# Kernel tuning notes

Measured on AMD Instinct MI355X. Metric: run time of the kernel, lower is better.

## Reference

```python
import jax, jax.numpy as jnp
import numpy as np
from jax import lax

B, T, V, LAT, U, P = 256, 128, 42, 200, 512, 3  # batch, seq, vocab, latent, lstm units, num_prop


def setup_inputs() -> dict:
    key = jax.random.key(0)
    ks = jax.random.split(key, 40)
    g = lambda i, shape, s=0.05: (jax.random.normal(ks[i], shape, jnp.float32) * s)
    inp = {
        'X': jax.random.randint(ks[0], (B, T), 0, V, jnp.int64 if jax.config.jax_enable_x64 else jnp.int32),
        'Y': jax.random.randint(ks[1], (B, T), 0, V, jnp.int32),
        'C': jax.random.normal(ks[2], (B, P), jnp.float32),
        'L': jax.random.randint(ks[3], (B,), 1, T + 1, jnp.int32),
        'eps': jax.random.normal(ks[4], (B, LAT), jnp.float32),
        'emb_enc': g(5, (V, LAT), 0.1),
        'emb_dec': g(6, (V, LAT), 0.1),
        # encoder stacked LSTM: layer0 input dim = LAT + P, layers 1-2 input dim = U
        'enc_k0': g(7, (LAT + P, 4 * U)), 'enc_rk0': g(8, (U, 4 * U)), 'enc_b0': jnp.zeros((4 * U,), jnp.float32),
        'enc_k1': g(9, (U, 4 * U)), 'enc_rk1': g(10, (U, 4 * U)), 'enc_b1': jnp.zeros((4 * U,), jnp.float32),
        'enc_k2': g(11, (U, 4 * U)), 'enc_rk2': g(12, (U, 4 * U)), 'enc_b2': jnp.zeros((4 * U,), jnp.float32),
        # decoder stacked LSTM: layer0 input dim = 2*LAT + P
        'dec_k0': g(13, (2 * LAT + P, 4 * U)), 'dec_rk0': g(14, (U, 4 * U)), 'dec_b0': jnp.zeros((4 * U,), jnp.float32),
        'dec_k1': g(15, (U, 4 * U)), 'dec_rk1': g(16, (U, 4 * U)), 'dec_b1': jnp.zeros((4 * U,), jnp.float32),
        'dec_k2': g(17, (U, 4 * U)), 'dec_rk2': g(18, (U, 4 * U)), 'dec_b2': jnp.zeros((4 * U,), jnp.float32),
        'Wm': g(19, (U, LAT)), 'bm': jnp.zeros((LAT,), jnp.float32),
        'Ws': g(20, (U, LAT)), 'bs': jnp.zeros((LAT,), jnp.float32),
        'Wo': g(21, (U, V)), 'bo': jnp.zeros((V,), jnp.float32),
    }
    return inp


def _lstm_step(x, h, c, k, rk, b):
    # Keras LSTMCell gate order: i, f, g(candidate), o
    z = x @ k + h @ rk + b
    i, f, gg, o = jnp.split(z, 4, axis=-1)
    c2 = jax.nn.sigmoid(f) * c + jax.nn.sigmoid(i) * jnp.tanh(gg)
    h2 = jax.nn.sigmoid(o) * jnp.tanh(c2)
    return h2, c2


def _run_stacked(inp, params):
    # inp: [B, T, D]; params: list of 3 (kernel, recurrent_kernel, bias)
    b = inp.shape[0]
    init = tuple((jnp.zeros((b, U), inp.dtype), jnp.zeros((b, U), inp.dtype)) for _ in range(3))

    def scan_fn(carry, x_t):
        h_in = x_t
        new = []
        for (h, c), (k, rk, bb) in zip(carry, params):
            h2, c2 = _lstm_step(h_in, h, c, k, rk, bb)
            new.append((h2, c2))
            h_in = h2
        return tuple(new), h_in

    carry, ys = lax.scan(scan_fn, init, jnp.swapaxes(inp, 0, 1))
    return jnp.swapaxes(ys, 0, 1), carry  # [B,T,U], final states


def reference(X, Y, C, L, eps, emb_enc, emb_dec,
              enc_k0, enc_rk0, enc_b0, enc_k1, enc_rk1, enc_b1, enc_k2, enc_rk2, enc_b2,
              dec_k0, dec_rk0, dec_b0, dec_k1, dec_rk1, dec_b1, dec_k2, dec_rk2, dec_b2,
              Wm, bm, Ws, bs, Wo, bo):
    enc_params = [(enc_k0, enc_rk0, enc_b0), (enc_k1, enc_rk1, enc_b1), (enc_k2, enc_rk2, enc_b2)]
    dec_params = [(dec_k0, dec_rk0, dec_b0), (dec_k1, dec_rk1, dec_b1), (dec_k2, dec_rk2, dec_b2)]

    # ---- encode ----
    Xe = emb_enc[X]                                       # [B,T,LAT]
    Ct = jnp.broadcast_to(C[:, None, :], (B, T, P))
    enc_in = jnp.concatenate([Xe, Ct], axis=-1)           # [B,T,LAT+P]
    _, enc_states = _run_stacked(enc_in, enc_params)
    h = enc_states[-1][1]                                 # CELL state of last layer (state[-1][1])
    mean = h @ Wm + bm
    log_sigma = h @ Ws + bs
    z = mean + jnp.exp(log_sigma / 2.0) * eps             # [B,LAT]

    # ---- decode ----
    Zt = jnp.broadcast_to(z[:, None, :], (B, T, LAT))
    Xd = emb_dec[X]
    dec_in = jnp.concatenate([Zt, Xd, Ct], axis=-1)       # [B,T,2*LAT+P]
    dec_out, _ = _run_stacked(dec_in, dec_params)
    pre = dec_out @ Wo + bo                               # pre-softmax logits [B,T,V]

    # ---- losses ----
    logp = jax.nn.log_softmax(pre, axis=-1)
    ce = -jnp.take_along_axis(logp, Y[..., None].astype(jnp.int32), axis=-1)[..., 0]  # [B,T]
    weights = (jnp.arange(T)[None, :] < L[:, None]).astype(jnp.float32)
    recon = jnp.mean(ce * weights)
    latent = -0.5 * jnp.mean(1.0 + log_sigma - jnp.square(mean) - jnp.exp(log_sigma))
    loss = recon + latent
    return loss, recon, latent
```

## Files before the change

### kernel.cpp

```cpp
#include <hip/hip_runtime.h>

#define B_ 256
#define T_ 128
#define V_ 42
#define LAT_ 200
#define U_ 512
#define G4_ 2048
#define NBLK 196
#define FI(r, m) ((((r) * 2) + (m)) * 32)
#define SLOT_ ((size_t)B_ * U_)
#define LS_ ((size_t)129 * SLOT_)

typedef unsigned short ushort_t;
typedef __attribute__((ext_vector_type(8))) short bf8;
typedef __attribute__((ext_vector_type(4))) float f4;

__device__ __forceinline__ ushort_t f2bf(float f) {
  union { float f; unsigned int i; } v; v.f = f;
  unsigned int r = v.i + 0x7fffu + ((v.i >> 16) & 1u);
  return (ushort_t)(r >> 16);
}
__device__ __forceinline__ float sigf(float x) { return 1.f / (1.f + __expf(-x)); }
__device__ __forceinline__ float tanhfast(float x) {
  float e = __expf(2.f * x);
  return 1.f - 2.f / (e + 1.f);
}
__device__ __forceinline__ void wait_vm0() {
  asm volatile("s_waitcnt vmcnt(0)" ::: "memory");
}

__global__ __launch_bounds__(256) void table_kernel(const float* emb, const float* k0, int roff, float* table) {
  int v = blockIdx.x, tid = threadIdx.x;
  __shared__ float e[LAT_];
  for (int i = tid; i < LAT_; i += 256) e[i] = emb[v * LAT_ + i];
  __syncthreads();
  for (int j = tid; j < G4_; j += 256) {
    float s = 0.f;
    for (int n = 0; n < LAT_; n++) s += e[n] * k0[(size_t)(roff + n) * G4_ + j];
    table[v * G4_ + j] = s;
  }
}

__device__ __forceinline__ size_t mat_off_u4(int m) {
  if (m == 0) return 0;
  if (m == 1) return 147456;
  if (m < 10) return 360448 + (size_t)(m - 2) * 131072;
  return 1409024;
}

struct SwzSrc {
  const float *enc_rk0, *enc_k0, *enc_b0;
  const float *dec_rk0, *dec_k0, *dec_b0;
  const float *tabE, *tabD;
  const float *encK1, *encR1, *encK2, *encR2;
  const float *decK1, *decR1, *decK2, *decR2;
  const float *Wo;
  ushort_t* dst;
};

__device__ float swz_val(const SwzSrc& s, int mat, int k, int n) {
  switch (mat) {
    case 0: {
      if (k < 512) return s.enc_rk0[(size_t)k * G4_ + n];
      int i = k - 512;
      if (i < 42) return s.tabE[(size_t)i * G4_ + n];
      if (i < 45) return s.enc_k0[(size_t)(200 + i - 42) * G4_ + n];
      if (i == 45) return s.enc_b0[n];
      return 0.f;
    }
    case 1: {
      if (k < 512) return s.dec_rk0[(size_t)k * G4_ + n];
      int i = k - 512;
      if (i < 200) return s.dec_k0[(size_t)i * G4_ + n];
      if (i < 256) return 0.f;
      i -= 256;
      if (i < 42) return s.tabD[(size_t)i * G4_ + n];
      if (i < 45) return s.dec_k0[(size_t)(400 + i - 42) * G4_ + n];
      if (i == 45) return s.dec_b0[n];
      return 0.f;
    }
    case 2: return s.encK1[(size_t)k * G4_ + n];
    case 3: return s.encR1[(size_t)k * G4_ + n];
    case 4: return s.encK2[(size_t)k * G4_ + n];
    case 5: return s.encR2[(size_t)k * G4_ + n];
    case 6: return s.decK1[(size_t)k * G4_ + n];
    case 7: return s.decR1[(size_t)k * G4_ + n];
    case 8: return s.decK2[(size_t)k * G4_ + n];
    case 9: return s.decR2[(size_t)k * G4_ + n];
    default: return (n < V_) ? s.Wo[(size_t)k * V_ + n] : 0.f;
  }
}

__global__ __launch_bounds__(256) void swz_ext_kernel(SwzSrc s) {
  int b = blockIdx.x, tid = threadIdx.x;
  int mat, nt16;
  if (b < 1280) { mat = b >> 7; nt16 = b & 127; } else { mat = 10; nt16 = b - 1280; }
  int ktMax = (mat == 0) ? 18 : (mat == 1) ? 26 : 16;
  int lane = tid & 63, l15 = lane & 15, q = lane >> 4;
  int n = nt16 * 16 + l15;
  uint4* dst = (uint4*)s.dst;
  size_t off = mat_off_u4(mat);
  for (int kt = tid >> 6; kt < ktMax; kt += 4) {
    ushort_t o[8];
    int kb = kt * 32 + q * 8;
#pragma unroll
    for (int j = 0; j < 8; j++) o[j] = f2bf(swz_val(s, mat, kb + j, n));
    dst[off + ((size_t)nt16 * ktMax + kt) * 64 + lane] = *(const uint4*)o;
  }
}

struct PP {
  const ushort_t* swz;
  ushort_t* ring;
  float* c2g; ushort_t* zf16; float* sums; int* bar; int* gen; int* flg; float* out;
  const float *enc_b1, *enc_b2, *dec_b1, *dec_b2;
  const float *Wm, *bm, *Ws, *bs, *eps, *C, *bo;
  const int *X, *Y, *Lb;
};

__device__ __forceinline__ void grid_barrier(int* bar, int* gen) {
  __builtin_amdgcn_fence(__ATOMIC_RELEASE, "agent");
  __syncthreads();
  if (threadIdx.x == 0) {
    int g = __hip_atomic_load(gen, __ATOMIC_RELAXED, __HIP_MEMORY_SCOPE_AGENT);
    if (__hip_atomic_fetch_add(bar, 1, __ATOMIC_ACQ_REL, __HIP_MEMORY_SCOPE_AGENT) == NBLK - 1) {
      __hip_atomic_store(bar, 0, __ATOMIC_RELAXED, __HIP_MEMORY_SCOPE_AGENT);
      __hip_atomic_store(gen, g + 1, __ATOMIC_RELEASE, __HIP_MEMORY_SCOPE_AGENT);
    } else {
      int gg;
      do {
        __builtin_amdgcn_s_sleep(1);
        gg = __hip_atomic_load(gen, __ATOMIC_ACQUIRE, __HIP_MEMORY_SCOPE_AGENT);
      } while (gg == g);
    }
  }
  __syncthreads();
  __builtin_amdgcn_fence(__ATOMIC_ACQUIRE, "agent");
}

__device__ __forceinline__ void wait_flags(const int* f, int cnt, int target) {
  int lane = threadIdx.x & 63;
  const int* a = f + (lane < cnt ? lane : 0);
  bool bad;
  do {
    int v = __hip_atomic_load(a, __ATOMIC_RELAXED, __HIP_MEMORY_SCOPE_AGENT);
    bad = (lane < cnt) && (v < target);
  } while (__ballot(bad) != 0ull);
}

#define MFMA(a, bfrag, c) __builtin_amdgcn_mfma_f32_16x16x32_bf16((a), (bfrag), (c), 0, 0, 0)

__global__ __launch_bounds__(256, 1) void persist(PP p) {
  __shared__ uint4 wlds4[8192];
  const int b = blockIdx.x, tid = threadIdx.x;
  const int lane = tid & 63, w = tid >> 6, q = lane >> 4, l15 = lane & 15;
  const int role = b < 64 ? 0 : b < 128 ? 1 : b < 192 ? 2 : 3;
  const int idx = b & 63;
  const int ut = idx >> 1;
  const int mi = idx & 1;
  const int m0 = mi * 128;
  const int rw = m0 + w * 32;
  const int u = ut * 16 + l15;
  const uint4* swzU4 = (const uint4*)p.swz;
  const int cb = b - 192;

  unsigned char* tok = (unsigned char*)wlds4 + 106496;
  unsigned char* ytok = (unsigned char*)wlds4 + 49152;

  ushort_t cb0[2][3];
  if (role == 0) {
#pragma unroll
    for (int ms = 0; ms < 2; ms++)
#pragma unroll
      for (int j = 0; j < 3; j++) cb0[ms][j] = f2bf(p.C[(rw + ms * 16 + l15) * 3 + j]);
  }

  const int pubidx = FI(role, mi) + ut;

  float ce_local = 0.f;
  float boR0 = 0.f, boR1 = 0.f, boR2 = 0.f;
  int Lr[4] = {0, 0, 0, 0};
  int pub = 0;

  for (int phase = 0; phase < 2; phase++) {
    const bool dec = (phase == 1);

    if (dec) {
      grid_barrier(p.bar, p.gen);
      if (b < 50) {
        int lat0 = b * 4;
        int row = tid;
        float m[4], ls[4];
#pragma unroll
        for (int lc = 0; lc < 4; lc++) { m[lc] = p.bm[lat0 + lc]; ls[lc] = p.bs[lat0 + lc]; }
        const float* cr = p.c2g + (size_t)row * U_;
        for (int k = 0; k < U_; k++) {
          float hv = cr[k];
#pragma unroll
          for (int lc = 0; lc < 4; lc++) {
            m[lc] += hv * p.Wm[k * LAT_ + lat0 + lc];
            ls[lc] += hv * p.Ws[k * LAT_ + lat0 + lc];
          }
        }
        float kl = 0.f;
#pragma unroll
        for (int lc = 0; lc < 4; lc++) {
          int lat = lat0 + lc;
          float zz = m[lc] + __expf(0.5f * ls[lc]) * p.eps[row * LAT_ + lat];
          p.zf16[row * 256 + lat] = f2bf(zz);
          kl += 1.f + ls[lc] - m[lc] * m[lc] - __expf(ls[lc]);
        }
        float* red = (float*)wlds4;
        red[tid] = kl; __syncthreads();
        for (int st = 128; st > 0; st >>= 1) { if (tid < st) red[tid] += red[tid + st]; __syncthreads(); }
        if (tid == 0) atomicAdd(p.sums + 1, red[0]);
      }
      __syncthreads();
    }

    if (role == 0) {
      if (!dec) {
        size_t mo = mat_off_u4(0);
        for (int g = 0; g < 4; g++) {
          int nt16 = g * 32 + ut;
          size_t src = mo + (size_t)nt16 * 18 * 64;
          int dst = g * 18 * 64;
          for (int i = tid; i < 18 * 64; i += 256) wlds4[dst + i] = swzU4[src + i];
        }
        for (int i = tid; i < 128 * T_; i += 256) {
          int r = i >> 7, t = i & 127;
          tok[r * 133 + t] = (unsigned char)p.X[(size_t)(m0 + r) * T_ + t];
        }
      } else {
        size_t mo = mat_off_u4(1);
        for (int g = 0; g < 4; g++) {
          int nt16 = g * 32 + ut;
          size_t src = mo + (size_t)nt16 * 26 * 64;
          int dst = g * 18 * 64;
          for (int i = tid; i < 16 * 64; i += 256) wlds4[dst + i] = swzU4[src + i];
          for (int i = tid; i < 2 * 64; i += 256) wlds4[dst + 16 * 64 + i] = swzU4[src + 24 * 64 + i];
          for (int i = tid; i < 8 * 64; i += 256) wlds4[4608 + g * 512 + i] = swzU4[src + 16 * 64 + i];
        }
      }
    } else if (role <= 2) {
      int matK = dec ? (role == 1 ? 6 : 8) : (role == 1 ? 2 : 4);
      for (int gm = 0; gm < 2; gm++) {
        size_t mo = mat_off_u4(matK + gm);
        for (int g = 0; g < 4; g++) {
          int nt16 = g * 32 + ut;
          size_t src = mo + (size_t)nt16 * 1024;
          int dst = gm * 4096 + g * 1024;
          for (int i = tid; i < 1024; i += 256) wlds4[dst + i] = swzU4[src + i];
        }
      }
    } else if (dec) {
      size_t mo = mat_off_u4(10);
      for (int i = tid; i < 3072; i += 256) wlds4[i] = swzU4[mo + i];
      for (int i = tid; i < 64 * T_; i += 256) {
        int r = i >> 7, t = i & 127;
        ytok[r * 133 + t] = (unsigned char)p.Y[(size_t)(cb * 64 + r) * T_ + t];
      }
      int r0c = cb * 64 + w * 16;
      boR0 = p.bo[l15]; boR1 = p.bo[16 + l15]; boR2 = (l15 < 10) ? p.bo[32 + l15] : 0.f;
#pragma unroll
      for (int r = 0; r < 4; r++) Lr[r] = p.Lb[r0c + q * 4 + r];
    }
    __syncthreads();

    float creg[2][4];
#pragma unroll
    for (int ms = 0; ms < 2; ms++)
#pragma unroll
      for (int r = 0; r < 4; r++) creg[ms][r] = 0.f;
    float bias[4] = {0.f, 0.f, 0.f, 0.f};
    if (role == 1 || role == 2) {
      const float* bb = dec ? (role == 1 ? p.dec_b1 : p.dec_b2) : (role == 1 ? p.enc_b1 : p.enc_b2);
#pragma unroll
      for (int g = 0; g < 4; g++) bias[g] = bb[g * 512 + u];
    }

    const int* myp = nullptr; int myc = 0;
    if (role == 0) {
      if (w == 0) { myp = p.flg + FI(0, mi); myc = 32; }
    } else if (role == 1) {
      if (w == 0) { myp = p.flg + FI(0, mi); myc = 32; }
      else if (w == 1) { myp = p.flg + FI(1, mi); myc = 32; }
    } else if (role == 2) {
      if (w == 0) { myp = p.flg + FI(1, mi); myc = 32; }
      else if (w == 1) { myp = p.flg + FI(2, mi); myc = 32; }
    } else {
      if (w == 0 && dec) { myp = p.flg + FI(2, cb >> 1); myc = 32; }
    }

    grid_barrier(p.bar, p.gen);

    f4 zacc[2][4];
#pragma unroll
    for (int ms = 0; ms < 2; ms++)
#pragma unroll
      for (int g = 0; g < 4; g++) zacc[ms][g] = (f4){0.f, 0.f, 0.f, 0.f};
    if (role == 0 && dec) {
      const ushort_t* Az0 = p.zf16 + (rw + l15) * 256 + q * 8;
#pragma unroll
      for (int kz = 0; kz < 8; kz++) {
        bf8 a0 = *(const bf8*)(Az0 + kz * 32);
        bf8 a1 = *(const bf8*)(Az0 + 16 * 256 + kz * 32);
#pragma unroll
        for (int g = 0; g < 4; g++) {
          bf8 bbf = *(const bf8*)&wlds4[4608 + g * 512 + kz * 64 + lane];
          zacc[0][g] = MFMA(a0, bbf, zacc[0][g]);
          zacc[1][g] = MFMA(a1, bbf, zacc[1][g]);
        }
      }
    }

    const int smax = dec ? T_ + 3 : T_ + 2;
    for (int s = 0; s < smax; s++) {
      pub++;
      if (myc) wait_flags(myp, myc, pub - 1);
      __syncthreads();

      const int lag = (role <= 2) ? role : 3;
      const int t = s - lag;
      if (role == 3) {
        if (dec && t >= 0 && t < T_) {
          int r0c = cb * 64 + w * 16;
          const ushort_t* Ar = p.ring + 2 * LS_ + (size_t)(t + 1) * SLOT_ + (size_t)(r0c + l15) * U_ + q * 8;
          f4 a3[3];
#pragma unroll
          for (int nt = 0; nt < 3; nt++) a3[nt] = (f4){0.f, 0.f, 0.f, 0.f};
#pragma unroll 4
          for (int kt = 0; kt < 16; kt++) {
            bf8 a = *(const bf8*)(Ar + kt * 32);
#pragma unroll
            for (int nt = 0; nt < 3; nt++) {
              bf8 bbf = *(const bf8*)&wlds4[nt * 1024 + kt * 64 + lane];
              a3[nt] = MFMA(a, bbf, a3[nt]);
            }
          }
#pragma unroll
          for (int r = 0; r < 4; r++) {
            float v0 = a3[0][r] + boR0;
            float v1 = a3[1][r] + boR1;
            float v2 = (l15 < 10) ? a3[2][r] + boR2 : -3.0e38f;
            float mx = fmaxf(fmaxf(v0, v1), v2);
            mx = fmaxf(mx, __shfl_xor(mx, 1)); mx = fmaxf(mx, __shfl_xor(mx, 2));
            mx = fmaxf(mx, __shfl_xor(mx, 4)); mx = fmaxf(mx, __shfl_xor(mx, 8));
            float se = __expf(v0 - mx) + __expf(v1 - mx) + ((l15 < 10) ? __expf(v2 - mx) : 0.f);
            int yv = ytok[(w * 16 + q * 4 + r) * 133 + t];
            float py = (l15 == yv ? v0 : 0.f) + (l15 + 16 == yv ? v1 : 0.f) + (l15 + 32 == yv ? v2 : 0.f);
            se += __shfl_xor(se, 1); se += __shfl_xor(se, 2); se += __shfl_xor(se, 4); se += __shfl_xor(se, 8);
            py += __shfl_xor(py, 1); py += __shfl_xor(py, 2); py += __shfl_xor(py, 4); py += __shfl_xor(py, 8);
            if (l15 == 0 && t < Lr[r]) ce_local += mx + __logf(se) - py;
          }
        }
      } else if (t >= 0 && t < T_) {
        f4 acc[2][4];
#pragma unroll
        for (int ms = 0; ms < 2; ms++)
#pragma unroll
          for (int g = 0; g < 4; g++) acc[ms][g] = zacc[ms][g];

        const ushort_t* hin = p.ring + (size_t)role * LS_ + (size_t)t * SLOT_;
        ushort_t* hout = p.ring + (size_t)role * LS_ + (size_t)(t + 1) * SLOT_;
        const ushort_t* Ah0 = hin + (size_t)(rw + l15) * U_ + q * 8;
        const ushort_t* Ah1 = Ah0 + 16 * U_;

        if (role == 0) {
          const int KT64 = 18 * 64;
#pragma unroll 4
          for (int kt = 0; kt < 16; kt++) {
            bf8 a0 = *(const bf8*)(Ah0 + kt * 32);
            bf8 a1 = *(const bf8*)(Ah1 + kt * 32);
#pragma unroll
            for (int g = 0; g < 4; g++) {
              bf8 bbf = *(const bf8*)&wlds4[g * KT64 + kt * 64 + lane];
              acc[0][g] = MFMA(a0, bbf, acc[0][g]);
              acc[1][g] = MFMA(a1, bbf, acc[1][g]);
            }
          }
          int xv0 = tok[(w * 32 + l15) * 133 + t];
          int xv1 = tok[(w * 32 + 16 + l15) * 133 + t];
#pragma unroll
          for (int ktc = 0; ktc < 2; ktc++) {
            union { ushort_t us[8]; bf8 v; } a0u, a1u;
#pragma unroll
            for (int j = 0; j < 8; j++) {
              int id = ktc * 32 + q * 8 + j;
              ushort_t v0 = (id == xv0) ? (ushort_t)0x3F80 : (ushort_t)0;
              ushort_t v1 = (id == xv1) ? (ushort_t)0x3F80 : (ushort_t)0;
              if (id >= 42 && id < 45) { v0 = cb0[0][id - 42]; v1 = cb0[1][id - 42]; }
              if (id == 45) { v0 = 0x3F80; v1 = 0x3F80; }
              a0u.us[j] = v0; a1u.us[j] = v1;
            }
            int kt = 16 + ktc;
#pragma unroll
            for (int g = 0; g < 4; g++) {
              bf8 bbf = *(const bf8*)&wlds4[g * KT64 + kt * 64 + lane];
              acc[0][g] = MFMA(a0u.v, bbf, acc[0][g]);
              acc[1][g] = MFMA(a1u.v, bbf, acc[1][g]);
            }
          }
        } else {
          const ushort_t* xin = p.ring + (size_t)(role - 1) * LS_ + (size_t)(t + 1) * SLOT_;
          const ushort_t* Ax0 = xin + (size_t)(rw + l15) * U_ + q * 8;
          const ushort_t* Ax1 = Ax0 + 16 * U_;
#pragma unroll 4
          for (int kt = 0; kt < 16; kt++) {
            bf8 a0 = *(const bf8*)(Ax0 + kt * 32);
            bf8 a1 = *(const bf8*)(Ax1 + kt * 32);
#pragma unroll
            for (int g = 0; g < 4; g++) {
              bf8 bbf = *(const bf8*)&wlds4[g * 1024 + kt * 64 + lane];
              acc[0][g] = MFMA(a0, bbf, acc[0][g]);
              acc[1][g] = MFMA(a1, bbf, acc[1][g]);
            }
          }
#pragma unroll 4
          for (int kt = 0; kt < 16; kt++) {
            bf8 a0 = *(const bf8*)(Ah0 + kt * 32);
            bf8 a1 = *(const bf8*)(Ah1 + kt * 32);
#pragma unroll
            for (int g = 0; g < 4; g++) {
              bf8 bbf = *(const bf8*)&wlds4[4096 + g * 1024 + kt * 64 + lane];
              acc[0][g] = MFMA(a0, bbf, acc[0][g]);
              acc[1][g] = MFMA(a1, bbf, acc[1][g]);
            }
          }
        }

#pragma unroll
        for (int ms = 0; ms < 2; ms++)
#pragma unroll
          for (int r = 0; r < 4; r++) {
            int row = rw + ms * 16 + q * 4 + r;
            float zi = acc[ms][0][r] + bias[0];
            float zf = acc[ms][1][r] + bias[1];
            float zg = acc[ms][2][r] + bias[2];
            float zo = acc[ms][3][r] + bias[3];
            float cp = creg[ms][r];
            float cn = sigf(zf) * cp + sigf(zi) * tanhfast(zg);
            float hn = sigf(zo) * tanhfast(cn);
            creg[ms][r] = cn;
            unsigned int part = (unsigned int)f2bf(hn);
            unsigned int up = (unsigned int)__shfl_xor((int)part, 1);
            if ((l15 & 1) == 0) {
              unsigned int packed = part | (up << 16);
              __hip_atomic_exchange((unsigned int*)&hout[(size_t)row * U_ + u], packed,
                                    __ATOMIC_RELAXED, __HIP_MEMORY_SCOPE_AGENT);
            }
            if (!dec && role == 2 && t == T_ - 1) p.c2g[(size_t)row * U_ + u] = cn;
          }
      }
      wait_vm0();
      __syncthreads();
      if (tid == 0 && role < 3)
        __hip_atomic_exchange(p.flg + pubidx, pub, __ATOMIC_RELAXED, __HIP_MEMORY_SCOPE_AGENT);
    }
  }

  if (role == 3 && l15 == 0) atomicAdd(p.sums + 0, ce_local);
  grid_barrier(p.bar, p.gen);
  if (b == 0 && tid == 0) {
    float recon = p.sums[0] * (1.f / ((float)B_ * (float)T_));
    float latent = -0.5f * p.sums[1] * (1.f / ((float)B_ * (float)LAT_));
    p.out[0] = recon + latent;
    p.out[1] = recon;
    p.out[2] = latent;
  }
}

extern "C" void kernel_launch(void* const* d_in, const int* in_sizes, int n_in,
                              void* d_out, int out_size, void* d_ws, size_t ws_size,
                              hipStream_t stream) {
  const int*   X       = (const int*)d_in[0];
  const int*   Y       = (const int*)d_in[1];
  const float* C       = (const float*)d_in[2];
  const int*   L       = (const int*)d_in[3];
  const float* eps     = (const float*)d_in[4];
  const float* emb_enc = (const float*)d_in[5];
  const float* emb_dec = (const float*)d_in[6];
  const float* enc_k0  = (const float*)d_in[7];
  const float* enc_rk0 = (const float*)d_in[8];
  const float* enc_b0  = (const float*)d_in[9];
  const float* enc_k1  = (const float*)d_in[10];
  const float* enc_rk1 = (const float*)d_in[11];
  const float* enc_b1  = (const float*)d_in[12];
  const float* enc_k2  = (const float*)d_in[13];
  const float* enc_rk2 = (const float*)d_in[14];
  const float* enc_b2  = (const float*)d_in[15];
  const float* dec_k0  = (const float*)d_in[16];
  const float* dec_rk0 = (const float*)d_in[17];
  const float* dec_b0  = (const float*)d_in[18];
  const float* dec_k1  = (const float*)d_in[19];
  const float* dec_rk1 = (const float*)d_in[20];
  const float* dec_b1  = (const float*)d_in[21];
  const float* dec_k2  = (const float*)d_in[22];
  const float* dec_rk2 = (const float*)d_in[23];
  const float* dec_b2  = (const float*)d_in[24];
  const float* Wm      = (const float*)d_in[25];
  const float* bm      = (const float*)d_in[26];
  const float* Ws      = (const float*)d_in[27];
  const float* bs      = (const float*)d_in[28];
  const float* Wo      = (const float*)d_in[29];
  const float* bo      = (const float*)d_in[30];
  float* out = (float*)d_out;
  (void)in_sizes; (void)n_in; (void)out_size; (void)ws_size;

  char* wsb = (char*)d_ws;
  size_t o = 0;
  auto take = [&](size_t bytes) -> char* { char* p = wsb + o; o += (bytes + 255) & ~(size_t)255; return p; };

  float* c2g  = (float*)take((size_t)B_ * U_ * 4);
  ushort_t* zf16 = (ushort_t*)take((size_t)B_ * 256 * 2);
  float* sums = (float*)take(8);
  int* bar = (int*)take(4);
  int* gen = (int*)take(4);
  int* flg = (int*)take(4 * 2 * 32 * 4);
  size_t zero_bytes = o;
  ushort_t* ring = (ushort_t*)take(3 * LS_ * 2);
  ushort_t* swz = (ushort_t*)take((size_t)1412096 * 16);
  float* tabE = (float*)take((size_t)V_ * G4_ * 4);
  float* tabD = (float*)take((size_t)V_ * G4_ * 4);

  hipMemsetAsync(wsb, 0, zero_bytes, stream);
  for (int l = 0; l < 3; l++)
    hipMemsetAsync(ring + (size_t)l * LS_, 0, SLOT_ * 2, stream);

  table_kernel<<<V_, 256, 0, stream>>>(emb_enc, enc_k0, 0, tabE);
  table_kernel<<<V_, 256, 0, stream>>>(emb_dec, dec_k0, 200, tabD);

  SwzSrc ss;
  ss.enc_rk0 = enc_rk0; ss.enc_k0 = enc_k0; ss.enc_b0 = enc_b0;
  ss.dec_rk0 = dec_rk0; ss.dec_k0 = dec_k0; ss.dec_b0 = dec_b0;
  ss.tabE = tabE; ss.tabD = tabD;
  ss.encK1 = enc_k1; ss.encR1 = enc_rk1; ss.encK2 = enc_k2; ss.encR2 = enc_rk2;
  ss.decK1 = dec_k1; ss.decR1 = dec_rk1; ss.decK2 = dec_k2; ss.decR2 = dec_rk2;
  ss.Wo = Wo; ss.dst = swz;
  swz_ext_kernel<<<1283, 256, 0, stream>>>(ss);

  PP pp;
  pp.swz = swz; pp.ring = ring;
  pp.c2g = c2g; pp.zf16 = zf16; pp.sums = sums; pp.bar = bar; pp.gen = gen; pp.flg = flg; pp.out = out;
  pp.enc_b1 = enc_b1; pp.enc_b2 = enc_b2; pp.dec_b1 = dec_b1; pp.dec_b2 = dec_b2;
  pp.Wm = Wm; pp.bm = bm; pp.Ws = Ws; pp.bs = bs; pp.eps = eps; pp.C = C; pp.bo = bo;
  pp.X = X; pp.Y = Y; pp.Lb = L;
  persist<<<NBLK, 256, 0, stream>>>(pp);
}
```

Measured before the change: 5.086 ms.

## Use write-through stores for h publish and flags, vectorize flag polling with backoff

Replaces the packed 32-bit atomic exchange of hidden-state values with per-element 16-bit write-through global stores (sc0 sc1), which removes the cross-lane shuffle. Flag publication likewise becomes a plain write-through dword store. The flag wait now reads two flags per lane with 64-bit loads and sleeps between polls, and the grid barrier spin sleeps longer. The aim is to cut atomic and polling traffic on the inter-block handoff path, at the cost of more store instructions and possibly higher wake-up latency from the longer sleeps.

```diff
diff --git a/kernel.cpp b/kernel.cpp
--- a/kernel.cpp
+++ b/kernel.cpp
@@ -27,6 +27,13 @@
 }
 __device__ __forceinline__ void wait_vm0() {
   asm volatile("s_waitcnt vmcnt(0)" ::: "memory");
+}
+__device__ __forceinline__ void st_wt_b16(void* p, ushort_t v) {
+  unsigned int vv = v;
+  asm volatile("global_store_short %0, %1, off sc0 sc1" :: "v"(p), "v"(vv) : "memory");
+}
+__device__ __forceinline__ void st_wt_b32(void* p, unsigned int v) {
+  asm volatile("global_store_dword %0, %1, off sc0 sc1" :: "v"(p), "v"(v) : "memory");
 }
 
 __global__ __launch_bounds__(256) void table_kernel(const float* emb, const float* k0, int roff, float* table) {
@@ -129,7 +136,7 @@
     } else {
       int gg;
       do {
-        __builtin_amdgcn_s_sleep(1);
+        __builtin_amdgcn_s_sleep(8);
         gg = __hip_atomic_load(gen, __ATOMIC_ACQUIRE, __HIP_MEMORY_SCOPE_AGENT);
       } while (gg == g);
     }
@@ -140,12 +147,14 @@
 
 __device__ __forceinline__ void wait_flags(const int* f, int cnt, int target) {
   int lane = threadIdx.x & 63;
-  const int* a = f + (lane < cnt ? lane : 0);
-  bool bad;
-  do {
-    int v = __hip_atomic_load(a, __ATOMIC_RELAXED, __HIP_MEMORY_SCOPE_AGENT);
-    bad = (lane < cnt) && (v < target);
-  } while (__ballot(bad) != 0ull);
+  bool need = (lane * 2) < cnt;
+  const unsigned long long* a = (const unsigned long long*)f + (need ? lane : 0);
+  for (;;) {
+    unsigned long long v = __hip_atomic_load(a, __ATOMIC_RELAXED, __HIP_MEMORY_SCOPE_AGENT);
+    bool bad = need && ((int)v < target || (int)(v >> 32) < target);
+    if (__ballot(bad) == 0ull) return;
+    __builtin_amdgcn_s_sleep(8);
+  }
 }
 
 #define MFMA(a, bfrag, c) __builtin_amdgcn_mfma_f32_16x16x32_bf16((a), (bfrag), (c), 0, 0, 0)
@@ -442,20 +451,13 @@
             float cn = sigf(zf) * cp + sigf(zi) * tanhfast(zg);
             float hn = sigf(zo) * tanhfast(cn);
             creg[ms][r] = cn;
-            unsigned int part = (unsigned int)f2bf(hn);
-            unsigned int up = (unsigned int)__shfl_xor((int)part, 1);
-            if ((l15 & 1) == 0) {
-              unsigned int packed = part | (up << 16);
-              __hip_atomic_exchange((unsigned int*)&hout[(size_t)row * U_ + u], packed,
-                                    __ATOMIC_RELAXED, __HIP_MEMORY_SCOPE_AGENT);
-            }
+            st_wt_b16(&hout[(size_t)row * U_ + u], f2bf(hn));
             if (!dec && role == 2 && t == T_ - 1) p.c2g[(size_t)row * U_ + u] = cn;
           }
       }
       wait_vm0();
       __syncthreads();
-      if (tid == 0 && role < 3)
-        __hip_atomic_exchange(p.flg + pubidx, pub, __ATOMIC_RELAXED, __HIP_MEMORY_SCOPE_AGENT);
+      if (tid == 0 && role < 3) st_wt_b32(p.flg + pubidx, (unsigned int)pub);
     }
   }
 
```

After: 5.388 ms. 5.9% more time.
